# Optimization experiments

Hardware: AMD Instinct MI355X
Metric: run time of the kernel (lower is better)

Reference implementation:

```python
import math
import jax, jax.numpy as jnp
import numpy as np

EMBED_DIM = 512
NUM_HEADS = 8
HEAD_DIM = EMBED_DIM // NUM_HEADS
NUM_EDGE_TYPES = 10
N = 2048  # nodes
B = 1


def setup_inputs() -> dict:
    key = jax.random.key(0)
    ks = jax.random.split(key, 8)
    s = 1.0 / math.sqrt(EMBED_DIM)
    return {
        "query": jax.random.normal(ks[0], (N, B, EMBED_DIM), jnp.float32),
        "key": jax.random.normal(ks[1], (N, B, EMBED_DIM), jnp.float32),
        "value": jax.random.normal(ks[2], (N, B, EMBED_DIM), jnp.float32),
        "edge_id_mat": jax.random.randint(ks[3], (N, N), 0, NUM_EDGE_TYPES, jnp.int32),
        "in_proj_weight": jax.random.normal(ks[4], (3 * EMBED_DIM, EMBED_DIM), jnp.float32) * s,
        "in_proj_bias": jnp.zeros((3 * EMBED_DIM,), jnp.float32),
        "out_proj_weight": jax.random.normal(ks[5], (EMBED_DIM, EMBED_DIM), jnp.float32) * s,
        "out_proj_bias": jnp.zeros((EMBED_DIM,), jnp.float32),
        "edge_embs_K": jax.random.normal(ks[6], (NUM_EDGE_TYPES, HEAD_DIM), jnp.float32),
    }


def reference(query, key, value, edge_id_mat, in_proj_weight, in_proj_bias,
              out_proj_weight, out_proj_bias, edge_embs_K):
    L, Bsz, E = query.shape
    H, hd = NUM_HEADS, HEAD_DIM
    w_q, w_k, w_v = jnp.split(in_proj_weight, 3, axis=0)
    b_q, b_k, b_v = jnp.split(in_proj_bias, 3)
    q = query @ w_q.T + b_q   # (L, B, E)
    k = key @ w_k.T + b_k
    v = value @ w_v.T + b_v

    def split_heads(x):
        # (L, B, E) -> (B*H, L, hd)  (matches torch view(L, B*H, hd).transpose(0,1))
        return x.reshape(L, Bsz * H, hd).transpose(1, 0, 2)

    q = split_heads(q) / math.sqrt(hd)  # torch scales by sqrt(E=head_dim)
    k = split_heads(k)
    v = split_heads(v)

    attn = jnp.einsum('bnd,bmd->bnm', q, k)  # (B*H, L, L)

    # edge-type score bias: edge_attn[b,i,j] = q[b,i,:] . edge_embs_K[edge_id_mat[i,j], :]
    # computed efficiently as per-type scores then a gather (avoids (L,L,hd) tensor)
    type_scores = jnp.einsum('bnd,td->bnt', q, edge_embs_K)  # (B*H, L, T)
    idx = jnp.broadcast_to(edge_id_mat[None, :, :], attn.shape)
    edge_attn = jnp.take_along_axis(type_scores, idx, axis=2)  # (B*H, L, L)
    attn = jax.nn.softmax(attn + edge_attn, axis=-1)

    out = jnp.einsum('bnm,bmd->bnd', attn, v)           # (B*H, L, hd)
    out = out.transpose(1, 0, 2).reshape(L, Bsz, E)      # (L, B, E)
    out = out @ out_proj_weight.T + out_proj_bias
    return out
```

## Files before the change

kernel.cpp:

```cpp
#include <hip/hip_runtime.h>
#include <hip/hip_bf16.h>

#define NHEAD 8
#define SEQ   2048
#define HD    64
#define EMB   512
#define NTYPE 10
#define JSPLIT 4

#define QKV_NT (3 * EMB / 64)
#define QKV_MT (SEQ / 64)
#define QKV_BLOCKS (QKV_NT * QKV_MT)
#define PACK_BLOCKS (SEQ * SEQ / 4 / 256)

#define QSCALE 0.180336878f

typedef unsigned short u16;
typedef __attribute__((ext_vector_type(8))) short short8;
typedef __attribute__((ext_vector_type(4))) float float4v;

union F8 { short8 v; uint4 u4; u16 us[8]; };

__device__ __forceinline__ float bf2f(u16 u){
  union { unsigned u; float f; } w; w.u = ((unsigned)u) << 16; return w.f;
}
__device__ __forceinline__ u16 f2bf(float f){
  union { float f; unsigned u; } w; w.f = f;
  unsigned u = w.u;
  u += 0x7fffu + ((u >> 16) & 1u);
  return (u16)(u >> 16);
}
__device__ __forceinline__ unsigned cvtpk(float lo, float hi){
  union { __hip_bfloat162 b; unsigned u; } w;
  w.b = __float22bfloat162_rn(float2{lo, hi});
  return w.u;
}
__device__ __forceinline__ uint4 pk8(float4 a, float4 b){
  uint4 p; p.x = cvtpk(a.x, a.y); p.y = cvtpk(a.z, a.w);
           p.z = cvtpk(b.x, b.y); p.w = cvtpk(b.z, b.w);
  return p;
}

__global__ __launch_bounds__(256) void fused_prep_gemm(
    const float* __restrict__ q, const float* __restrict__ k, const float* __restrict__ v,
    const float* __restrict__ ipw, const float* __restrict__ ipb, const int* __restrict__ eid,
    u16* __restrict__ Qs, u16* __restrict__ Kb, u16* __restrict__ Vb,
    unsigned* __restrict__ eidp)
{
  const int b = blockIdx.x;
  const int t = threadIdx.x;

  if (b >= QKV_BLOCKS) {
    const int i = (b - QKV_BLOCKS) * 256 + t;
    int4 vv = ((const int4*)eid)[i];
    eidp[i] = (unsigned)(vv.x & 0xff) | ((unsigned)(vv.y & 0xff) << 8) |
              ((unsigned)(vv.z & 0xff) << 16) | ((unsigned)(vv.w & 0xff) << 24);
    return;
  }

  __shared__ u16 As[64][40];
  __shared__ u16 Bs[64][40];

  const int nt = b % QKV_NT, mt = b / QKV_NT;
  const int n0 = nt * 64, m0 = mt * 64;
  const int z = n0 >> 9;
  const float* A = (z == 0) ? q : (z == 1) ? k : v;
  const float scale = (z == 0) ? QSCALE : 1.0f;

  const int w = t >> 6, lane = t & 63, lr = lane & 15, lg = lane >> 4;
  const int wm = w >> 1, wn = w & 1;
  const int srow = t >> 2, kb = (t & 3) * 8;

  float4v acc[2][2];
#pragma unroll
  for (int mi = 0; mi < 2; mi++)
#pragma unroll
    for (int ni = 0; ni < 2; ni++) acc[mi][ni] = (float4v){0.f, 0.f, 0.f, 0.f};

  const float* pa = A   + (size_t)(m0 + srow) * EMB + kb;
  const float* pw = ipw + (size_t)(n0 + srow) * EMB + kb;

  float4 a0 = *(const float4*)pa, a1 = *(const float4*)(pa + 4);
  float4 b0 = *(const float4*)pw, b1 = *(const float4*)(pw + 4);

  for (int k0 = 0; k0 < EMB; k0 += 32) {
    *(uint4*)&As[srow][kb] = pk8(a0, a1);
    *(uint4*)&Bs[srow][kb] = pk8(b0, b1);
    __syncthreads();
    if (k0 + 32 < EMB) {
      a0 = *(const float4*)(pa + k0 + 32); a1 = *(const float4*)(pa + k0 + 36);
      b0 = *(const float4*)(pw + k0 + 32); b1 = *(const float4*)(pw + k0 + 36);
    }
    F8 af[2], bf_[2];
#pragma unroll
    for (int mi = 0; mi < 2; mi++)
      af[mi].u4 = *(const uint4*)&As[wm * 32 + mi * 16 + lr][lg * 8];
#pragma unroll
    for (int ni = 0; ni < 2; ni++)
      bf_[ni].u4 = *(const uint4*)&Bs[wn * 32 + ni * 16 + lr][lg * 8];
#pragma unroll
    for (int mi = 0; mi < 2; mi++)
#pragma unroll
      for (int ni = 0; ni < 2; ni++)
        acc[mi][ni] = __builtin_amdgcn_mfma_f32_16x16x32_bf16(af[mi].v, bf_[ni].v, acc[mi][ni], 0, 0, 0);
    __syncthreads();
  }

  u16* O = (z == 0) ? Qs : ((z == 1) ? Kb : Vb);
#pragma unroll
  for (int mi = 0; mi < 2; mi++) {
#pragma unroll
    for (int ni = 0; ni < 2; ni++) {
      const int n = n0 + wn * 32 + ni * 16 + lr;
      const int e = n & 511, h = e >> 6, d = e & 63;
      const float bb = ipb[n];
      const int mb = m0 + wm * 32 + mi * 16 + lg * 4;
      if (z < 2) {
#pragma unroll
        for (int r = 0; r < 4; r++)
          O[((size_t)h * SEQ + mb + r) * HD + d] = f2bf((acc[mi][ni][r] + bb) * scale);
      } else {
        ushort4 pk;
        pk.x = f2bf(acc[mi][ni][0] + bb); pk.y = f2bf(acc[mi][ni][1] + bb);
        pk.z = f2bf(acc[mi][ni][2] + bb); pk.w = f2bf(acc[mi][ni][3] + bb);
        *(ushort4*)(O + ((size_t)(h * HD + d)) * SEQ + mb) = pk;
      }
    }
  }
}

__global__ __launch_bounds__(256) void attn_kernel(
    const u16* __restrict__ Qs, const u16* __restrict__ Kb, const u16* __restrict__ Vb,
    const unsigned* __restrict__ eid32, const float* __restrict__ EK,
    float* __restrict__ Upart, float* __restrict__ mpart, float* __restrict__ lpart)
{
  __shared__ u16 Kt[64][72];
  __shared__ u16 Vt[64][72];
  __shared__ u16 Pl[4][16][72];
  __shared__ float tsl[64][13];
  __shared__ float ekl[NTYPE][64];

  const int t = threadIdx.x;
  const int wave = t >> 6, lane = t & 63, lr = lane & 15, lg = lane >> 4;
  const int i0 = blockIdx.x * 64;
  const int h  = blockIdx.y;
  const int z  = blockIdx.z;

  for (int i = t; i < NTYPE * 64; i += 256) ekl[i >> 6][i & 63] = EK[i];
  __syncthreads();

  {
    const int row = t >> 2, tt = t & 3;
    const u16* qr = Qs + ((size_t)h * SEQ + i0 + row) * HD;
    float a0 = 0.f, a1 = 0.f, a2 = 0.f;
    for (int d0 = 0; d0 < HD; d0 += 8) {
      uint4 qq = *(const uint4*)(qr + d0);
      const u16* qu = (const u16*)&qq;
#pragma unroll
      for (int e = 0; e < 8; e++) {
        float qf = bf2f(qu[e]);
        a0 += qf * ekl[tt][d0 + e];
        a1 += qf * ekl[tt + 4][d0 + e];
        a2 += qf * ekl[(tt < 2) ? (tt + 8) : 8][d0 + e];
      }
    }
    tsl[row][tt] = a0; tsl[row][tt + 4] = a1;
    if (tt < 2) tsl[row][tt + 8] = a2;
  }

  F8 qf[2];
#pragma unroll
  for (int kc = 0; kc < 2; kc++)
    qf[kc].u4 = *(const uint4*)(Qs + ((size_t)h * SEQ + i0 + wave * 16 + lr) * HD + kc * 32 + lg * 8);

  float4v ao[4];
#pragma unroll
  for (int d = 0; d < 4; d++) ao[d] = (float4v){0.f, 0.f, 0.f, 0.f};
  float m_i = -1e30f, l_i = 0.f;

  const int srow = t >> 2, sdc = (t & 3) * 16;
  const int jbase = z * (SEQ / JSPLIT);
  const int NT = (SEQ / JSPLIT) / 64;
  const unsigned* erow = eid32 + (size_t)(i0 + wave * 16 + lr) * (SEQ / 4);

  uint4 kp0, kp1, vp0, vp1;
  unsigned ed[4], edn[4];
  {
    const u16* kp = Kb + ((size_t)h * SEQ + jbase + srow) * HD + sdc;
    kp0 = *(const uint4*)kp; kp1 = *(const uint4*)(kp + 8);
    const u16* vp = Vb + ((size_t)(h * HD + srow)) * SEQ + jbase + sdc;
    vp0 = *(const uint4*)vp; vp1 = *(const uint4*)(vp + 8);
    *(uint4*)&Kt[srow][sdc] = kp0; *(uint4*)&Kt[srow][sdc + 8] = kp1;
    *(uint4*)&Vt[srow][sdc] = vp0; *(uint4*)&Vt[srow][sdc + 8] = vp1;
    const int ej = jbase >> 2;
#pragma unroll
    for (int c = 0; c < 4; c++) ed[c] = erow[ej + c * 4 + lg];
  }

  for (int jt = 0; jt < NT; jt++) {
    __syncthreads();

    if (jt + 1 < NT) {
      const int jn = jbase + (jt + 1) * 64;
      const u16* kp = Kb + ((size_t)h * SEQ + jn + srow) * HD + sdc;
      kp0 = *(const uint4*)kp; kp1 = *(const uint4*)(kp + 8);
      const u16* vp = Vb + ((size_t)(h * HD + srow)) * SEQ + jn + sdc;
      vp0 = *(const uint4*)vp; vp1 = *(const uint4*)(vp + 8);
      const int ejn = jn >> 2;
#pragma unroll
      for (int c = 0; c < 4; c++) edn[c] = erow[ejn + c * 4 + lg];
    }

    float4v sacc[4];
#pragma unroll
    for (int c = 0; c < 4; c++) sacc[c] = (float4v){0.f, 0.f, 0.f, 0.f};
#pragma unroll
    for (int kc = 0; kc < 2; kc++) {
#pragma unroll
      for (int c = 0; c < 4; c++) {
        F8 kf; kf.u4 = *(const uint4*)&Kt[c * 16 + lr][kc * 32 + lg * 8];
        sacc[c] = __builtin_amdgcn_mfma_f32_16x16x32_bf16(kf.v, qf[kc].v, sacc[c], 0, 0, 0);
      }
    }

    float rmax = -1e30f;
#pragma unroll
    for (int c = 0; c < 4; c++) {
      const unsigned e = ed[c];
#pragma unroll
      for (int r = 0; r < 4; r++) {
        const float s = sacc[c][r] + tsl[wave * 16 + lr][(e >> (r * 8)) & 0xffu];
        sacc[c][r] = s;
        rmax = fmaxf(rmax, s);
      }
    }
    rmax = fmaxf(rmax, __shfl_xor(rmax, 16));
    rmax = fmaxf(rmax, __shfl_xor(rmax, 32));
    const float mnew = fmaxf(m_i, rmax);
    const float fct = exp2f(m_i - mnew);
    float rsum = 0.f;
#pragma unroll
    for (int c = 0; c < 4; c++) {
#pragma unroll
      for (int r = 0; r < 4; r++) {
        const float p = exp2f(sacc[c][r] - mnew);
        sacc[c][r] = p;
        rsum += p;
      }
    }
    rsum += __shfl_xor(rsum, 16);
    rsum += __shfl_xor(rsum, 32);
    l_i = l_i * fct + rsum;
    m_i = mnew;

#pragma unroll
    for (int c = 0; c < 4; c++) {
      uint2 pw;
      pw.x = cvtpk(sacc[c][0], sacc[c][1]);
      pw.y = cvtpk(sacc[c][2], sacc[c][3]);
      *(uint2*)&Pl[wave][lr][c * 16 + lg * 4] = pw;
    }
#pragma unroll
    for (int db = 0; db < 4; db++) {
#pragma unroll
      for (int r = 0; r < 4; r++) ao[db][r] *= fct;
    }
#pragma unroll
    for (int kc = 0; kc < 2; kc++) {
      F8 pf; pf.u4 = *(const uint4*)&Pl[wave][lr][kc * 32 + lg * 8];
#pragma unroll
      for (int db = 0; db < 4; db++) {
        F8 vf; vf.u4 = *(const uint4*)&Vt[db * 16 + lr][kc * 32 + lg * 8];
        ao[db] = __builtin_amdgcn_mfma_f32_16x16x32_bf16(vf.v, pf.v, ao[db], 0, 0, 0);
      }
    }

    __syncthreads();
    if (jt + 1 < NT) {
      *(uint4*)&Kt[srow][sdc] = kp0; *(uint4*)&Kt[srow][sdc + 8] = kp1;
      *(uint4*)&Vt[srow][sdc] = vp0; *(uint4*)&Vt[srow][sdc + 8] = vp1;
#pragma unroll
      for (int c = 0; c < 4; c++) ed[c] = edn[c];
    }
  }

  {
    const size_t base = (((size_t)z * NHEAD + h) * SEQ + i0) * HD;
#pragma unroll
    for (int db = 0; db < 4; db++) {
#pragma unroll
      for (int r = 0; r < 4; r++) {
        const int d = db * 16 + lg * 4 + r;
        const int n = wave * 16 + lr;
        Upart[base + (size_t)n * HD + d] = ao[db][r];
      }
    }
    if (lg == 0) {
      mpart[((size_t)z * NHEAD + h) * SEQ + i0 + wave * 16 + lr] = m_i;
      lpart[((size_t)z * NHEAD + h) * SEQ + i0 + wave * 16 + lr] = l_i;
    }
  }
}

__global__ __launch_bounds__(256) void combine_outproj(
    const float* __restrict__ Upart, const float* __restrict__ mpart,
    const float* __restrict__ lpart, const float* __restrict__ opw,
    const float* __restrict__ opb, float* __restrict__ out)
{
  __shared__ u16 As[64][40];
  __shared__ u16 Bs[64][40];
  __shared__ float cww[JSPLIT][NHEAD][64];

  const int t = threadIdx.x;
  const int n0 = blockIdx.x * 64;
  const int m0 = blockIdx.y * 64;

  for (int idx = t; idx < NHEAD * 64; idx += 256) {
    const int hh = idx >> 6, nl = idx & 63;
    const int gn = m0 + nl;
    float mz[JSPLIT], wz[JSPLIT];
    float M = -1e30f;
#pragma unroll
    for (int zz = 0; zz < JSPLIT; zz++) {
      mz[zz] = mpart[((size_t)zz * NHEAD + hh) * SEQ + gn];
      M = fmaxf(M, mz[zz]);
    }
    float Ls = 0.f;
#pragma unroll
    for (int zz = 0; zz < JSPLIT; zz++) {
      wz[zz] = exp2f(mz[zz] - M);
      Ls += wz[zz] * lpart[((size_t)zz * NHEAD + hh) * SEQ + gn];
    }
    const float inv = 1.0f / Ls;
#pragma unroll
    for (int zz = 0; zz < JSPLIT; zz++) cww[zz][hh][nl] = wz[zz] * inv;
  }
  __syncthreads();

  const int w = t >> 6, lane = t & 63, lr = lane & 15, lg = lane >> 4;
  const int wm = w >> 1, wn = w & 1;
  const int srow = t >> 2, kb = (t & 3) * 8;

  float4v acc[2][2];
#pragma unroll
  for (int mi = 0; mi < 2; mi++)
#pragma unroll
    for (int ni = 0; ni < 2; ni++) acc[mi][ni] = (float4v){0.f, 0.f, 0.f, 0.f};

  const float* pw = opw + (size_t)(n0 + srow) * EMB + kb;

  int hcur = kb >> 6, dcur = kb & 63;
  float4 ua[JSPLIT][2];
#pragma unroll
  for (int zz = 0; zz < JSPLIT; zz++) {
    const float* pu = Upart + (((size_t)zz * NHEAD + hcur) * SEQ + m0 + srow) * HD + dcur;
    ua[zz][0] = *(const float4*)pu; ua[zz][1] = *(const float4*)(pu + 4);
  }
  float4 b0 = *(const float4*)pw, b1 = *(const float4*)(pw + 4);

  for (int k0 = 0; k0 < EMB; k0 += 32) {
    {
      float4 c0 = {0.f,0.f,0.f,0.f}, c1 = {0.f,0.f,0.f,0.f};
#pragma unroll
      for (int zz = 0; zz < JSPLIT; zz++) {
        const float wgt = cww[zz][hcur][srow];
        c0.x += ua[zz][0].x * wgt; c0.y += ua[zz][0].y * wgt;
        c0.z += ua[zz][0].z * wgt; c0.w += ua[zz][0].w * wgt;
        c1.x += ua[zz][1].x * wgt; c1.y += ua[zz][1].y * wgt;
        c1.z += ua[zz][1].z * wgt; c1.w += ua[zz][1].w * wgt;
      }
      *(uint4*)&As[srow][kb] = pk8(c0, c1);
      *(uint4*)&Bs[srow][kb] = pk8(b0, b1);
    }
    __syncthreads();
    if (k0 + 32 < EMB) {
      const int e = k0 + 32 + kb;
      hcur = e >> 6; dcur = e & 63;
#pragma unroll
      for (int zz = 0; zz < JSPLIT; zz++) {
        const float* pu = Upart + (((size_t)zz * NHEAD + hcur) * SEQ + m0 + srow) * HD + dcur;
        ua[zz][0] = *(const float4*)pu; ua[zz][1] = *(const float4*)(pu + 4);
      }
      b0 = *(const float4*)(pw + k0 + 32); b1 = *(const float4*)(pw + k0 + 36);
    }
    F8 af[2], bf_[2];
#pragma unroll
    for (int mi = 0; mi < 2; mi++)
      af[mi].u4 = *(const uint4*)&As[wm * 32 + mi * 16 + lr][lg * 8];
#pragma unroll
    for (int ni = 0; ni < 2; ni++)
      bf_[ni].u4 = *(const uint4*)&Bs[wn * 32 + ni * 16 + lr][lg * 8];
#pragma unroll
    for (int mi = 0; mi < 2; mi++)
#pragma unroll
      for (int ni = 0; ni < 2; ni++)
        acc[mi][ni] = __builtin_amdgcn_mfma_f32_16x16x32_bf16(af[mi].v, bf_[ni].v, acc[mi][ni], 0, 0, 0);
    __syncthreads();
  }

#pragma unroll
  for (int mi = 0; mi < 2; mi++) {
#pragma unroll
    for (int ni = 0; ni < 2; ni++) {
      const int n = n0 + wn * 32 + ni * 16 + lr;
      const float bb = opb[n];
      const int mb = m0 + wm * 32 + mi * 16 + lg * 4;
#pragma unroll
      for (int r = 0; r < 4; r++)
        out[(size_t)(mb + r) * EMB + n] = acc[mi][ni][r] + bb;
    }
  }
}

extern "C" void kernel_launch(void* const* d_in, const int* in_sizes, int n_in,
                              void* d_out, int out_size, void* d_ws, size_t ws_size,
                              hipStream_t stream)
{
  const float* query = (const float*)d_in[0];
  const float* key_  = (const float*)d_in[1];
  const float* value = (const float*)d_in[2];
  const int*   eid   = (const int*)d_in[3];
  const float* ipw   = (const float*)d_in[4];
  const float* ipb   = (const float*)d_in[5];
  const float* opw   = (const float*)d_in[6];
  const float* opb   = (const float*)d_in[7];
  const float* ek    = (const float*)d_in[8];
  float* out = (float*)d_out;

  char* ws = (char*)d_ws;
  u16* Qs = (u16*)ws;              ws += (size_t)NHEAD * SEQ * HD * 2;
  u16* Kb = (u16*)ws;              ws += (size_t)NHEAD * SEQ * HD * 2;
  u16* Vb = (u16*)ws;              ws += (size_t)NHEAD * SEQ * HD * 2;
  unsigned* eidp = (unsigned*)ws;  ws += (size_t)SEQ * SEQ;
  float* Upart = (float*)ws;       ws += (size_t)JSPLIT * NHEAD * SEQ * HD * 4;
  float* mpart = (float*)ws;       ws += (size_t)JSPLIT * NHEAD * SEQ * 4;
  float* lpart = (float*)ws;       ws += (size_t)JSPLIT * NHEAD * SEQ * 4;

  fused_prep_gemm<<<dim3(QKV_BLOCKS + PACK_BLOCKS), dim3(256), 0, stream>>>(
      query, key_, value, ipw, ipb, eid, Qs, Kb, Vb, eidp);
  attn_kernel<<<dim3(SEQ / 64, NHEAD, JSPLIT), dim3(256), 0, stream>>>(
      Qs, Kb, Vb, eidp, ek, Upart, mpart, lpart);
  combine_outproj<<<dim3(EMB / 64, SEQ / 64), dim3(256), 0, stream>>>(
      Upart, mpart, lpart, opw, opb, out);
}
```

Before: 165.0 us.

## Store split-K attention partials as bf16 and deepen GEMM K-tiles to 64

The attention kernel now writes its per-split unnormalized outputs as packed bf16 with vectorized stores, where before it used scattered fp32 scalar stores. The combine/out-projection kernel reads them back as bf16. This halves the intermediate partial traffic, which is about 16MB in fp32. Both projection GEMMs also move from a K-step of 32 to 64, halving the number of barrier-synchronized iterations, at the cost of more LDS and registers. The partials are rounded to bf16 before the combine, which adds some precision loss.

```diff
diff --git a/kernel.cpp b/kernel.cpp
--- a/kernel.cpp
+++ b/kernel.cpp
@@ -58,8 +58,8 @@
     return;
   }
 
-  __shared__ u16 As[64][40];
-  __shared__ u16 Bs[64][40];
+  __shared__ u16 As[64][72];
+  __shared__ u16 Bs[64][72];
 
   const int nt = b % QKV_NT, mt = b / QKV_NT;
   const int n0 = nt * 64, m0 = mt * 64;
@@ -69,7 +69,7 @@
 
   const int w = t >> 6, lane = t & 63, lr = lane & 15, lg = lane >> 4;
   const int wm = w >> 1, wn = w & 1;
-  const int srow = t >> 2, kb = (t & 3) * 8;
+  const int srow = t >> 2, kb16 = (t & 3) * 16;
 
   float4v acc[2][2];
 #pragma unroll
@@ -77,32 +77,43 @@
 #pragma unroll
     for (int ni = 0; ni < 2; ni++) acc[mi][ni] = (float4v){0.f, 0.f, 0.f, 0.f};
 
-  const float* pa = A   + (size_t)(m0 + srow) * EMB + kb;
-  const float* pw = ipw + (size_t)(n0 + srow) * EMB + kb;
-
-  float4 a0 = *(const float4*)pa, a1 = *(const float4*)(pa + 4);
-  float4 b0 = *(const float4*)pw, b1 = *(const float4*)(pw + 4);
-
-  for (int k0 = 0; k0 < EMB; k0 += 32) {
-    *(uint4*)&As[srow][kb] = pk8(a0, a1);
-    *(uint4*)&Bs[srow][kb] = pk8(b0, b1);
-    __syncthreads();
-    if (k0 + 32 < EMB) {
-      a0 = *(const float4*)(pa + k0 + 32); a1 = *(const float4*)(pa + k0 + 36);
-      b0 = *(const float4*)(pw + k0 + 32); b1 = *(const float4*)(pw + k0 + 36);
-    }
-    F8 af[2], bf_[2];
-#pragma unroll
-    for (int mi = 0; mi < 2; mi++)
-      af[mi].u4 = *(const uint4*)&As[wm * 32 + mi * 16 + lr][lg * 8];
-#pragma unroll
-    for (int ni = 0; ni < 2; ni++)
-      bf_[ni].u4 = *(const uint4*)&Bs[wn * 32 + ni * 16 + lr][lg * 8];
-#pragma unroll
-    for (int mi = 0; mi < 2; mi++)
+  const float* pa = A   + (size_t)(m0 + srow) * EMB + kb16;
+  const float* pw = ipw + (size_t)(n0 + srow) * EMB + kb16;
+
+  float4 a[4], bb[4];
+#pragma unroll
+  for (int j = 0; j < 4; j++) { a[j] = *(const float4*)(pa + j * 4); bb[j] = *(const float4*)(pw + j * 4); }
+
+  for (int k0 = 0; k0 < EMB; k0 += 64) {
+    *(uint4*)&As[srow][kb16]     = pk8(a[0], a[1]);
+    *(uint4*)&As[srow][kb16 + 8] = pk8(a[2], a[3]);
+    *(uint4*)&Bs[srow][kb16]     = pk8(bb[0], bb[1]);
+    *(uint4*)&Bs[srow][kb16 + 8] = pk8(bb[2], bb[3]);
+    __syncthreads();
+    if (k0 + 64 < EMB) {
+#pragma unroll
+      for (int j = 0; j < 4; j++) {
+        a[j]  = *(const float4*)(pa + k0 + 64 + j * 4);
+        bb[j] = *(const float4*)(pw + k0 + 64 + j * 4);
+      }
+    }
+    F8 af[2][2], bf_[2][2];
+#pragma unroll
+    for (int kc = 0; kc < 2; kc++) {
+#pragma unroll
+      for (int mi = 0; mi < 2; mi++)
+        af[mi][kc].u4 = *(const uint4*)&As[wm * 32 + mi * 16 + lr][kc * 32 + lg * 8];
 #pragma unroll
       for (int ni = 0; ni < 2; ni++)
-        acc[mi][ni] = __builtin_amdgcn_mfma_f32_16x16x32_bf16(af[mi].v, bf_[ni].v, acc[mi][ni], 0, 0, 0);
+        bf_[ni][kc].u4 = *(const uint4*)&Bs[wn * 32 + ni * 16 + lr][kc * 32 + lg * 8];
+    }
+#pragma unroll
+    for (int kc = 0; kc < 2; kc++)
+#pragma unroll
+      for (int mi = 0; mi < 2; mi++)
+#pragma unroll
+        for (int ni = 0; ni < 2; ni++)
+          acc[mi][ni] = __builtin_amdgcn_mfma_f32_16x16x32_bf16(af[mi][kc].v, bf_[ni][kc].v, acc[mi][ni], 0, 0, 0);
     __syncthreads();
   }
 
@@ -113,16 +124,16 @@
     for (int ni = 0; ni < 2; ni++) {
       const int n = n0 + wn * 32 + ni * 16 + lr;
       const int e = n & 511, h = e >> 6, d = e & 63;
-      const float bb = ipb[n];
+      const float bias = ipb[n];
       const int mb = m0 + wm * 32 + mi * 16 + lg * 4;
       if (z < 2) {
 #pragma unroll
         for (int r = 0; r < 4; r++)
-          O[((size_t)h * SEQ + mb + r) * HD + d] = f2bf((acc[mi][ni][r] + bb) * scale);
+          O[((size_t)h * SEQ + mb + r) * HD + d] = f2bf((acc[mi][ni][r] + bias) * scale);
       } else {
         ushort4 pk;
-        pk.x = f2bf(acc[mi][ni][0] + bb); pk.y = f2bf(acc[mi][ni][1] + bb);
-        pk.z = f2bf(acc[mi][ni][2] + bb); pk.w = f2bf(acc[mi][ni][3] + bb);
+        pk.x = f2bf(acc[mi][ni][0] + bias); pk.y = f2bf(acc[mi][ni][1] + bias);
+        pk.z = f2bf(acc[mi][ni][2] + bias); pk.w = f2bf(acc[mi][ni][3] + bias);
         *(ushort4*)(O + ((size_t)(h * HD + d)) * SEQ + mb) = pk;
       }
     }
@@ -132,7 +143,7 @@
 __global__ __launch_bounds__(256) void attn_kernel(
     const u16* __restrict__ Qs, const u16* __restrict__ Kb, const u16* __restrict__ Vb,
     const unsigned* __restrict__ eid32, const float* __restrict__ EK,
-    float* __restrict__ Upart, float* __restrict__ mpart, float* __restrict__ lpart)
+    u16* __restrict__ Upart, float* __restrict__ mpart, float* __restrict__ lpart)
 {
   __shared__ u16 Kt[64][72];
   __shared__ u16 Vt[64][72];
@@ -286,29 +297,28 @@
 
   {
     const size_t base = (((size_t)z * NHEAD + h) * SEQ + i0) * HD;
+    const int n = wave * 16 + lr;
 #pragma unroll
     for (int db = 0; db < 4; db++) {
-#pragma unroll
-      for (int r = 0; r < 4; r++) {
-        const int d = db * 16 + lg * 4 + r;
-        const int n = wave * 16 + lr;
-        Upart[base + (size_t)n * HD + d] = ao[db][r];
-      }
+      uint2 pw;
+      pw.x = cvtpk(ao[db][0], ao[db][1]);
+      pw.y = cvtpk(ao[db][2], ao[db][3]);
+      *(uint2*)(Upart + base + (size_t)n * HD + db * 16 + lg * 4) = pw;
     }
     if (lg == 0) {
-      mpart[((size_t)z * NHEAD + h) * SEQ + i0 + wave * 16 + lr] = m_i;
-      lpart[((size_t)z * NHEAD + h) * SEQ + i0 + wave * 16 + lr] = l_i;
+      mpart[((size_t)z * NHEAD + h) * SEQ + i0 + n] = m_i;
+      lpart[((size_t)z * NHEAD + h) * SEQ + i0 + n] = l_i;
     }
   }
 }
 
 __global__ __launch_bounds__(256) void combine_outproj(
-    const float* __restrict__ Upart, const float* __restrict__ mpart,
+    const u16* __restrict__ Upart, const float* __restrict__ mpart,
     const float* __restrict__ lpart, const float* __restrict__ opw,
     const float* __restrict__ opb, float* __restrict__ out)
 {
-  __shared__ u16 As[64][40];
-  __shared__ u16 Bs[64][40];
+  __shared__ u16 As[64][72];
+  __shared__ u16 Bs[64][72];
   __shared__ float cww[JSPLIT][NHEAD][64];
 
   const int t = threadIdx.x;
@@ -339,7 +349,7 @@
 
   const int w = t >> 6, lane = t & 63, lr = lane & 15, lg = lane >> 4;
   const int wm = w >> 1, wn = w & 1;
-  const int srow = t >> 2, kb = (t & 3) * 8;
+  const int srow = t >> 2, kb16 = (t & 3) * 16;
 
   float4v acc[2][2];
 #pragma unroll
@@ -347,54 +357,70 @@
 #pragma unroll
     for (int ni = 0; ni < 2; ni++) acc[mi][ni] = (float4v){0.f, 0.f, 0.f, 0.f};
 
-  const float* pw = opw + (size_t)(n0 + srow) * EMB + kb;
-
-  int hcur = kb >> 6, dcur = kb & 63;
-  float4 ua[JSPLIT][2];
+  const float* pw = opw + (size_t)(n0 + srow) * EMB + kb16;
+
+  int hcur = kb16 >> 6, dcur = kb16 & 63;
+  uint4 ua[JSPLIT][2];
 #pragma unroll
   for (int zz = 0; zz < JSPLIT; zz++) {
-    const float* pu = Upart + (((size_t)zz * NHEAD + hcur) * SEQ + m0 + srow) * HD + dcur;
-    ua[zz][0] = *(const float4*)pu; ua[zz][1] = *(const float4*)(pu + 4);
-  }
-  float4 b0 = *(const float4*)pw, b1 = *(const float4*)(pw + 4);
-
-  for (int k0 = 0; k0 < EMB; k0 += 32) {
+    const u16* pu = Upart + (((size_t)zz * NHEAD + hcur) * SEQ + m0 + srow) * HD + dcur;
+    ua[zz][0] = *(const uint4*)pu; ua[zz][1] = *(const uint4*)(pu + 8);
+  }
+  float4 bb[4];
+#pragma unroll
+  for (int j = 0; j < 4; j++) bb[j] = *(const float4*)(pw + j * 4);
+
+  for (int k0 = 0; k0 < EMB; k0 += 64) {
     {
-      float4 c0 = {0.f,0.f,0.f,0.f}, c1 = {0.f,0.f,0.f,0.f};
+      float cc[16];
+#pragma unroll
+      for (int j = 0; j < 16; j++) cc[j] = 0.f;
 #pragma unroll
       for (int zz = 0; zz < JSPLIT; zz++) {
         const float wgt = cww[zz][hcur][srow];
-        c0.x += ua[zz][0].x * wgt; c0.y += ua[zz][0].y * wgt;
-        c0.z += ua[zz][0].z * wgt; c0.w += ua[zz][0].w * wgt;
-        c1.x += ua[zz][1].x * wgt; c1.y += ua[zz][1].y * wgt;
-        c1.z += ua[zz][1].z * wgt; c1.w += ua[zz][1].w * wgt;
-      }
-      *(uint4*)&As[srow][kb] = pk8(c0, c1);
-      *(uint4*)&Bs[srow][kb] = pk8(b0, b1);
-    }
-    __syncthreads();
-    if (k0 + 32 < EMB) {
-      const int e = k0 + 32 + kb;
+        F8 q0, q1; q0.u4 = ua[zz][0]; q1.u4 = ua[zz][1];
+#pragma unroll
+        for (int j = 0; j < 8; j++) {
+          cc[j]     += wgt * bf2f((u16)q0.us[j]);
+          cc[j + 8] += wgt * bf2f((u16)q1.us[j]);
+        }
+      }
+      float4 c0 = {cc[0], cc[1], cc[2], cc[3]},   c1 = {cc[4], cc[5], cc[6], cc[7]};
+      float4 c2 = {cc[8], cc[9], cc[10], cc[11]}, c3 = {cc[12], cc[13], cc[14], cc[15]};
+      *(uint4*)&As[srow][kb16]     = pk8(c0, c1);
+      *(uint4*)&As[srow][kb16 + 8] = pk8(c2, c3);
+      *(uint4*)&Bs[srow][kb16]     = pk8(bb[0], bb[1]);
+      *(uint4*)&Bs[srow][kb16 + 8] = pk8(bb[2], bb[3]);
+    }
+    __syncthreads();
+    if (k0 + 64 < EMB) {
+      const int e = k0 + 64 + kb16;
       hcur = e >> 6; dcur = e & 63;
 #pragma unroll
       for (int zz = 0; zz < JSPLIT; zz++) {
-        const float* pu = Upart + (((size_t)zz * NHEAD + hcur) * SEQ + m0 + srow) * HD + dcur;
-        ua[zz][0] = *(const float4*)pu; ua[zz][1] = *(const float4*)(pu + 4);
-      }
-      b0 = *(const float4*)(pw + k0 + 32); b1 = *(const float4*)(pw + k0 + 36);
-    }
-    F8 af[2], bf_[2];
-#pragma unroll
-    for (int mi = 0; mi < 2; mi++)
-      af[mi].u4 = *(const uint4*)&As[wm * 32 + mi * 16 + lr][lg * 8];
-#pragma unroll
-    for (int ni = 0; ni < 2; ni++)
-      bf_[ni].u4 = *(const uint4*)&Bs[wn * 32 + ni * 16 + lr][lg * 8];
-#pragma unroll
-    for (int mi = 0; mi < 2; mi++)
+        const u16* pu = Upart + (((size_t)zz * NHEAD + hcur) * SEQ + m0 + srow) * HD + dcur;
+        ua[zz][0] = *(const uint4*)pu; ua[zz][1] = *(const uint4*)(pu + 8);
+      }
+#pragma unroll
+      for (int j = 0; j < 4; j++) bb[j] = *(const float4*)(pw + k0 + 64 + j * 4);
+    }
+    F8 af[2][2], bf_[2][2];
+#pragma unroll
+    for (int kc = 0; kc < 2; kc++) {
+#pragma unroll
+      for (int mi = 0; mi < 2; mi++)
+        af[mi][kc].u4 = *(const uint4*)&As[wm * 32 + mi * 16 + lr][kc * 32 + lg * 8];
 #pragma unroll
       for (int ni = 0; ni < 2; ni++)
-        acc[mi][ni] = __builtin_amdgcn_mfma_f32_16x16x32_bf16(af[mi].v, bf_[ni].v, acc[mi][ni], 0, 0, 0);
+        bf_[ni][kc].u4 = *(const uint4*)&Bs[wn * 32 + ni * 16 + lr][kc * 32 + lg * 8];
+    }
+#pragma unroll
+    for (int kc = 0; kc < 2; kc++)
+#pragma unroll
+      for (int mi = 0; mi < 2; mi++)
+#pragma unroll
+        for (int ni = 0; ni < 2; ni++)
+          acc[mi][ni] = __builtin_amdgcn_mfma_f32_16x16x32_bf16(af[mi][kc].v, bf_[ni][kc].v, acc[mi][ni], 0, 0, 0);
     __syncthreads();
   }
 
@@ -403,11 +429,11 @@
 #pragma unroll
     for (int ni = 0; ni < 2; ni++) {
       const int n = n0 + wn * 32 + ni * 16 + lr;
-      const float bb = opb[n];
+      const float bias = opb[n];
       const int mb = m0 + wm * 32 + mi * 16 + lg * 4;
 #pragma unroll
       for (int r = 0; r < 4; r++)
-        out[(size_t)(mb + r) * EMB + n] = acc[mi][ni][r] + bb;
+        out[(size_t)(mb + r) * EMB + n] = acc[mi][ni][r] + bias;
     }
   }
 }
@@ -432,7 +458,7 @@
   u16* Kb = (u16*)ws;              ws += (size_t)NHEAD * SEQ * HD * 2;
   u16* Vb = (u16*)ws;              ws += (size_t)NHEAD * SEQ * HD * 2;
   unsigned* eidp = (unsigned*)ws;  ws += (size_t)SEQ * SEQ;
-  float* Upart = (float*)ws;       ws += (size_t)JSPLIT * NHEAD * SEQ * HD * 4;
+  u16* Upart = (u16*)ws;           ws += (size_t)JSPLIT * NHEAD * SEQ * HD * 2;
   float* mpart = (float*)ws;       ws += (size_t)JSPLIT * NHEAD * SEQ * 4;
   float* lpart = (float*)ws;       ws += (size_t)JSPLIT * NHEAD * SEQ * 4;
 
```

After: 158.9 us. 1.04x faster.
